# Optimization experiments

Measured on AMD Instinct MI355X. Metric: run time of the kernel, lower is better.

Reference implementation:

```python
import jax, jax.numpy as jnp
import numpy as np

B, T, DIM = 512, 243, 512
C = DIM // 2      # 256 channels per branch
CH = C // 2       # 128 hidden channels in ECL (cdiv=2)


def layer_norm(x, g, b, eps=1e-5):
    m = jnp.mean(x, axis=-1, keepdims=True)
    v = jnp.var(x, axis=-1, keepdims=True)
    return (x - m) * jax.lax.rsqrt(v + eps) * g + b


def gconv(x_btc, w):
    # grouped conv1d (groups=2), kernel 3, pad 1, no bias; x: [B,T,Cin], w: [Cout, Cin//2, 3]
    x = jnp.transpose(x_btc, (0, 2, 1))  # NCH
    y = jax.lax.conv_general_dilated(
        x, w, window_strides=(1,), padding=[(1, 1)],
        dimension_numbers=('NCH', 'OIH', 'NCH'), feature_group_count=2)
    return jnp.transpose(y, (0, 2, 1))


def setup_inputs() -> dict:
    key = jax.random.key(0)
    ks = jax.random.split(key, 4)
    F = (T + 1) // 2  # 122 == T//2+1 for odd T
    return {
        'x': jax.random.normal(ks[0], (B, T, DIM), dtype=jnp.float32),
        'lfilter': jax.random.normal(ks[1], (F, T // 2 + 1, 2), dtype=jnp.float32) * 0.02,
        'w1': jax.random.normal(ks[2], (CH, C // 2, 3), dtype=jnp.float32) * 0.05,
        'w2': jax.random.normal(ks[3], (C, CH // 2, 3), dtype=jnp.float32) * 0.05,
        'g1': jnp.ones((CH,), jnp.float32),
        'b1': jnp.zeros((CH,), jnp.float32),
        'g2': jnp.ones((C,), jnp.float32),
        'b2': jnp.zeros((C,), jnp.float32),
    }


def reference(x, lfilter, w1, w2, g1, b1, g2, b2):
    res, gate = jnp.split(x, 2, axis=-1)  # each [B, T, C]
    # GlobalFilter: rfft -> learned complex matmul over frequency axis -> irfft
    X = jnp.fft.rfft(res.astype(jnp.float32), n=T, axis=1, norm='ortho')  # [B, T//2+1, C] complex
    lf = lfilter[..., 0] + 1j * lfilter[..., 1]  # [(T+1)//2, T//2+1]
    X = jnp.einsum('fk,bkc->bfc', lf, X)
    res = jnp.fft.irfft(X, n=T, axis=1, norm='ortho')  # [B, T, C]
    # ECL gating branch
    h = gconv(gate, w1)                                  # [B, T, CH]
    h = jax.nn.gelu(layer_norm(h, g1, b1), approximate=False)
    h = gconv(h, w2)                                     # [B, T, C]
    h = jax.nn.sigmoid(layer_norm(h, g2, b2))
    gate = gate * h
    return jnp.concatenate([res, gate], axis=-1)
```

## Files before the change

kernel.cpp:

```cpp
#include <hip/hip_runtime.h>
#include <math.h>

typedef unsigned short ushort_t;
typedef unsigned int uint_t;
typedef __attribute__((ext_vector_type(8))) short short8v;
typedef __attribute__((ext_vector_type(4))) float f32x4;

#define BB   512
#define TT   243
#define DIMV 512
#define CC   256
#define CHH  128
#define FF   122
#define NKK  122

__device__ __forceinline__ float b2f(ushort_t u) {
  union { uint_t i; float f; } z; z.i = ((uint_t)u) << 16; return z.f;
}
__device__ __forceinline__ ushort_t f2b(float f) {
  union { float f; uint_t i; } z; z.f = f;
  uint_t r = (z.i + 0x7fffu + ((z.i >> 16) & 1u)) >> 16;
  return (ushort_t)r;
}
__device__ __forceinline__ uint_t pack2(float a, float b) {
  uint_t r;
  asm("v_cvt_pk_bf16_f32 %0, %1, %2" : "=v"(r) : "v"(a), "v"(b));
  return r;
}
__device__ __forceinline__ float gelu_f(float x) {
  float z = fabsf(x) * 0.70710678118654752f;
  float t = __builtin_amdgcn_rcpf(fmaf(0.3275911f, z, 1.0f));
  float p = fmaf(1.061405429f, t, -1.453152027f);
  p = fmaf(p, t, 1.421413741f);
  p = fmaf(p, t, -0.284496736f);
  p = fmaf(p, t, 0.254829592f);
  p = p * t;
  float e = __expf(-z * z);
  float erfa = 1.0f - p * e;
  float erfs = copysignf(erfa, x);
  return 0.5f * x * (1.0f + erfs);
}
__device__ __forceinline__ float sigmoid_f(float x) {
  return __builtin_amdgcn_rcpf(1.0f + __expf(-x));
}
union FragU { uint_t u[4]; short8v s; };


__global__ void k_compute_A(const float* __restrict__ lf, float* __restrict__ A) {
  __shared__ float2 tab[TT];
  int f = blockIdx.x;
  int tp = threadIdx.x;
  if (tp < TT) {
    float s, c;
    sincosf(6.28318530717958647692f * (float)tp / (float)TT, &s, &c);
    tab[tp] = make_float2(s, c);
  }
  __syncthreads();
  if (tp >= TT) return;
  float are = 0.f, aim = 0.f;
  int m = 0;
  const float* lrow = lf + (size_t)f * NKK * 2;
  for (int k = 0; k < NKK; ++k) {
    float2 sc = tab[m];
    float lr = lrow[2 * k], li = lrow[2 * k + 1];
    are = fmaf(lr, sc.y, fmaf(li, sc.x, are));
    aim = fmaf(li, sc.y, fmaf(-lr, sc.x, aim));
    m += tp; if (m >= TT) m -= TT;
  }
  A[(f * TT + tp) * 2 + 0] = are;
  A[(f * TT + tp) * 2 + 1] = aim;
}

__global__ void k_compute_M(const float* __restrict__ A, ushort_t* __restrict__ Ffrag) {
  __shared__ float2 tab[TT];
  int t = blockIdx.x;
  int tp = threadIdx.x;
  if (tp < TT) {
    float s, c;
    sincosf(6.28318530717958647692f * (float)tp / (float)TT, &s, &c);
    tab[tp] = make_float2(s, c);
  }
  __syncthreads();
  float val = 0.f;
  if (t < TT && tp < TT) {
    float acc = A[tp * 2 + 0];
    int m = t;
    for (int f = 1; f < FF; ++f) {
      float2 sc = tab[m];
      float ar = A[(f * TT + tp) * 2 + 0];
      float ai = A[(f * TT + tp) * 2 + 1];
      acc = fmaf(2.f * ar, sc.y, fmaf(-2.f * ai, sc.x, acc));
      m += t; if (m >= TT) m -= TT;
    }
    val = acc * (1.0f / (float)TT);
  }
  int kstep = tp >> 5, ko = tp & 31, p = ko >> 3, j = ko & 7;
  int mt = t >> 4, row = t & 15, lane = p * 16 + row;
  Ffrag[(((kstep * 16 + mt) * 64) + lane) * 8 + j] = f2b(val);
}

__global__ void k_prep_w(const float* __restrict__ w1, const float* __restrict__ w2,
                         ushort_t* __restrict__ w1f, ushort_t* __restrict__ w2f) {
  int q = blockIdx.x * 256 + threadIdx.x;
  if (q < 49152) {
    int j = q & 7, l = (q >> 3) & 63, ot = (q >> 9) & 3, rest = q >> 11;
    int ks = rest % 12, g = rest / 12;
    int o = ot * 16 + (l & 15);
    int k = ks * 32 + 8 * (l >> 4) + j;
    int dk = k >> 7, i = k & 127;
    w1f[q] = f2b(w1[(g * 64 + o) * 384 + i * 3 + dk]);
  } else if (q < 98304) {
    int q2 = q - 49152;
    int j = q2 & 7, l = (q2 >> 3) & 63, ot = (q2 >> 9) & 7, rest = q2 >> 12;
    int ks = rest % 6, g = rest / 6;
    int o = ot * 16 + (l & 15);
    int k = ks * 32 + 8 * (l >> 4) + j;
    int dk = k >> 6, i = k & 63;
    w2f[q2] = f2b(w2[(g * 128 + o) * 192 + i * 3 + dk]);
  }
}


#define RST 17
__global__ __launch_bounds__(256) void k_res(const float* __restrict__ x,
    const ushort_t* __restrict__ Ffrag, float* __restrict__ out) {
  __shared__ uint_t xs[2][64 * RST];
  int b = blockIdx.x >> 2, c0 = (blockIdx.x & 3) * 64;
  int tid = threadIdx.x, l = tid & 63, w = tid >> 6;
  const float* xb = x + (size_t)b * TT * DIMV + c0;
  const short8v* Fp = (const short8v*)Ffrag;

  f32x4 acc[4][4];
#pragma unroll
  for (int q = 0; q < 4; ++q)
#pragma unroll
    for (int m = 0; m < 4; ++m) acc[q][m] = (f32x4){0.f, 0.f, 0.f, 0.f};

  float v0[4], v1[4];
  int cc = tid & 63, kp0 = tid >> 6;

#pragma unroll
  for (int it = 0; it < 4; ++it) {
    int kp = kp0 + 4 * it, tp = 2 * kp;
    v0[it] = (tp < TT) ? xb[(size_t)tp * DIMV + cc] : 0.f;
    v1[it] = (tp + 1 < TT) ? xb[(size_t)(tp + 1) * DIMV + cc] : 0.f;
  }
#pragma unroll
  for (int it = 0; it < 4; ++it) xs[0][cc * RST + kp0 + 4 * it] = pack2(v0[it], v1[it]);
  __syncthreads();

  for (int ks = 0; ks < 8; ++ks) {
    int cur = ks & 1;
    if (ks < 7) {
#pragma unroll
      for (int it = 0; it < 4; ++it) {
        int kp = kp0 + 4 * it, tp = (ks + 1) * 32 + 2 * kp;
        v0[it] = (tp < TT) ? xb[(size_t)tp * DIMV + cc] : 0.f;
        v1[it] = (tp + 1 < TT) ? xb[(size_t)(tp + 1) * DIMV + cc] : 0.f;
      }
    }
    FragU bfr[4];
#pragma unroll
    for (int q = 0; q < 4; ++q) bfr[q].s = Fp[(ks * 16 + 4 * w + q) * 64 + l];
#pragma unroll
    for (int m = 0; m < 4; ++m) {
      FragU af;
      const uint_t* pp = &xs[cur][(16 * m + (l & 15)) * RST + 4 * (l >> 4)];
      af.u[0] = pp[0]; af.u[1] = pp[1]; af.u[2] = pp[2]; af.u[3] = pp[3];
#pragma unroll
      for (int q = 0; q < 4; ++q)
        acc[q][m] = __builtin_amdgcn_mfma_f32_16x16x32_bf16(af.s, bfr[q].s, acc[q][m], 0, 0, 0);
    }
    if (ks < 7) {
#pragma unroll
      for (int it = 0; it < 4; ++it) xs[cur ^ 1][cc * RST + kp0 + 4 * it] = pack2(v0[it], v1[it]);
    }
    __syncthreads();
  }

  float* ob = out + (size_t)b * TT * DIMV + c0;
#pragma unroll
  for (int q = 0; q < 4; ++q) {
    int t = (4 * w + q) * 16 + (l & 15);
    if (t < TT) {
#pragma unroll
      for (int m = 0; m < 4; ++m)
        *(f32x4*)&ob[(size_t)t * DIMV + 16 * m + 4 * (l >> 4)] = acc[q][m];
    }
  }
}


#define BT    32
#define NTIL  8
#define XROWS 36
#define XSTD  132
#define HROWS 34
#define HSTD  68

__global__ __launch_bounds__(256) void k_gate(const float* __restrict__ x,
    const ushort_t* __restrict__ w1f, const float* __restrict__ g1, const float* __restrict__ b1,
    const ushort_t* __restrict__ w2f, const float* __restrict__ g2, const float* __restrict__ b2,
    float* __restrict__ out) {
  __shared__ uint_t xs[XROWS * XSTD];
  __shared__ uint_t hs[HROWS * HSTD];
  __shared__ float red1s[4][48], red1q[4][48];
  __shared__ float red2s[4][32], red2q[4][32];
  int b = blockIdx.x >> 3, t0 = (blockIdx.x & 7) * BT;
  int tid = threadIdx.x, l = tid & 63, w = tid >> 6;
  int g = w >> 1, half = w & 1;

  const float* xb = x + (size_t)b * TT * DIMV + CC;
#pragma unroll 3
  for (int it = 0; it < 9; ++it) {
    int e = tid + it * 256;
    int r = e >> 6, cq = e & 63;
    int t = t0 - 2 + r;
    float4 v = make_float4(0.f, 0.f, 0.f, 0.f);
    if (t >= 0 && t < TT) v = *(const float4*)&xb[(size_t)t * DIMV + 4 * cq];
    *(uint2*)&xs[r * XSTD + 2 * cq] = make_uint2(pack2(v.x, v.y), pack2(v.z, v.w));
  }
  __syncthreads();

  const short8v* w1p = (const short8v*)w1f;
  int gdw = g * 64;
  f32x4 acc1[2][3];
#pragma unroll
  for (int a = 0; a < 2; ++a)
#pragma unroll
    for (int nt = 0; nt < 3; ++nt) acc1[a][nt] = (f32x4){0.f, 0.f, 0.f, 0.f};

  for (int ks = 0; ks < 12; ++ks) {
    short8v af[2];
#pragma unroll
    for (int a = 0; a < 2; ++a)
      af[a] = w1p[((g * 12 + ks) * 4 + half * 2 + a) * 64 + l];
    int dk = ks >> 2, i0dw = (ks & 3) * 16;
    FragU bf[3];
#pragma unroll
    for (int nt = 0; nt < 3; ++nt) {
      int row = (l & 15) + 16 * nt + dk;
      if (nt == 2) row = row > (XROWS - 1) ? (XROWS - 1) : row;
      const uint4* pp = (const uint4*)&xs[row * XSTD + gdw + i0dw + 4 * (l >> 4)];
      uint4 qv = *pp;
      bf[nt].u[0] = qv.x; bf[nt].u[1] = qv.y; bf[nt].u[2] = qv.z; bf[nt].u[3] = qv.w;
    }
#pragma unroll
    for (int a = 0; a < 2; ++a)
#pragma unroll
      for (int nt = 0; nt < 3; ++nt)
        acc1[a][nt] = __builtin_amdgcn_mfma_f32_16x16x32_bf16(af[a], bf[nt].s, acc1[a][nt], 0, 0, 0);
  }

#pragma unroll
  for (int nt = 0; nt < 3; ++nt) {
    float s = 0.f, s2 = 0.f;
#pragma unroll
    for (int a = 0; a < 2; ++a)
#pragma unroll
      for (int r = 0; r < 4; ++r) { float v = acc1[a][nt][r]; s += v; s2 += v * v; }
    s += __shfl_xor(s, 16); s += __shfl_xor(s, 32);
    s2 += __shfl_xor(s2, 16); s2 += __shfl_xor(s2, 32);
    if (l < 16) { red1s[w][l + 16 * nt] = s; red1q[w][l + 16 * nt] = s2; }
  }
  __syncthreads();

#pragma unroll
  for (int nt = 0; nt < 3; ++nt) {
    int c = (l & 15) + 16 * nt;
    if (c < HROWS) {
      int t_out = t0 - 1 + c;
      bool valid = (t_out >= 0 && t_out < TT);
      float S = red1s[0][c] + red1s[1][c] + red1s[2][c] + red1s[3][c];
      float S2 = red1q[0][c] + red1q[1][c] + red1q[2][c] + red1q[3][c];
      float mean = S * (1.f / 128.f);
      float var = S2 * (1.f / 128.f) - mean * mean;
      float rstd = rsqrtf(var + 1e-5f);
#pragma unroll
      for (int a = 0; a < 2; ++a) {
        int o0 = g * 64 + half * 32 + a * 16 + 4 * (l >> 4);
        float4 gg = *(const float4*)&g1[o0];
        float4 bb = *(const float4*)&b1[o0];
        float gv[4] = {gg.x, gg.y, gg.z, gg.w};
        float bv[4] = {bb.x, bb.y, bb.z, bb.w};
        float h4[4];
#pragma unroll
        for (int r = 0; r < 4; ++r) {
          float xn = (acc1[a][nt][r] - mean) * rstd * gv[r] + bv[r];
          h4[r] = valid ? gelu_f(xn) : 0.f;
        }
        *(uint2*)&hs[c * HSTD + (o0 >> 1)] =
            make_uint2(pack2(h4[0], h4[1]), pack2(h4[2], h4[3]));
      }
    }
  }
  __syncthreads();

  const short8v* w2p = (const short8v*)w2f;
  int gdw2 = g * 32;
  f32x4 acc2[4][2];
#pragma unroll
  for (int a = 0; a < 4; ++a)
#pragma unroll
    for (int nt = 0; nt < 2; ++nt) acc2[a][nt] = (f32x4){0.f, 0.f, 0.f, 0.f};

  for (int ks = 0; ks < 6; ++ks) {
    short8v af[4];
#pragma unroll
    for (int a = 0; a < 4; ++a)
      af[a] = w2p[((g * 6 + ks) * 8 + half * 4 + a) * 64 + l];
    int dk = ks >> 1, i0dw = (ks & 1) * 16;
    FragU bf[2];
#pragma unroll
    for (int nt = 0; nt < 2; ++nt) {
      int row = (l & 15) + 16 * nt + dk;
      const uint4* pp = (const uint4*)&hs[row * HSTD + gdw2 + i0dw + 4 * (l >> 4)];
      uint4 qv = *pp;
      bf[nt].u[0] = qv.x; bf[nt].u[1] = qv.y; bf[nt].u[2] = qv.z; bf[nt].u[3] = qv.w;
    }
#pragma unroll
    for (int a = 0; a < 4; ++a)
#pragma unroll
      for (int nt = 0; nt < 2; ++nt)
        acc2[a][nt] = __builtin_amdgcn_mfma_f32_16x16x32_bf16(af[a], bf[nt].s, acc2[a][nt], 0, 0, 0);
  }

#pragma unroll
  for (int nt = 0; nt < 2; ++nt) {
    float s = 0.f, s2 = 0.f;
#pragma unroll
    for (int a = 0; a < 4; ++a)
#pragma unroll
      for (int r = 0; r < 4; ++r) { float v = acc2[a][nt][r]; s += v; s2 += v * v; }
    s += __shfl_xor(s, 16); s += __shfl_xor(s, 32);
    s2 += __shfl_xor(s2, 16); s2 += __shfl_xor(s2, 32);
    if (l < 16) { red2s[w][l + 16 * nt] = s; red2q[w][l + 16 * nt] = s2; }
  }
  __syncthreads();

  float* ob = out + (size_t)b * TT * DIMV + CC;
#pragma unroll
  for (int nt = 0; nt < 2; ++nt) {
    int c = (l & 15) + 16 * nt;
    int t = t0 + c;
    if (t < TT) {
      float S = red2s[0][c] + red2s[1][c] + red2s[2][c] + red2s[3][c];
      float S2 = red2q[0][c] + red2q[1][c] + red2q[2][c] + red2q[3][c];
      float mean = S * (1.f / 256.f);
      float var = S2 * (1.f / 256.f) - mean * mean;
      float rstd = rsqrtf(var + 1e-5f);
      int xrow = c + 2;
#pragma unroll
      for (int a = 0; a < 4; ++a) {
        int o0 = g * 128 + (half * 4 + a) * 16 + 4 * (l >> 4);
        float4 gg = *(const float4*)&g2[o0];
        float4 bb = *(const float4*)&b2[o0];
        float gv[4] = {gg.x, gg.y, gg.z, gg.w};
        float bv[4] = {bb.x, bb.y, bb.z, bb.w};
        uint2 xv2 = *(const uint2*)&xs[xrow * XSTD + (o0 >> 1)];
        float xvv[4] = { b2f((ushort_t)(xv2.x & 0xffff)), b2f((ushort_t)(xv2.x >> 16)),
                         b2f((ushort_t)(xv2.y & 0xffff)), b2f((ushort_t)(xv2.y >> 16)) };
        f32x4 res;
#pragma unroll
        for (int r = 0; r < 4; ++r) {
          float xn = (acc2[a][nt][r] - mean) * rstd * gv[r] + bv[r];
          res[r] = xvv[r] * sigmoid_f(xn);
        }
        *(f32x4*)&ob[(size_t)t * DIMV + o0] = res;
      }
    }
  }
}


extern "C" void kernel_launch(void* const* d_in, const int* in_sizes, int n_in,
                              void* d_out, int out_size, void* d_ws, size_t ws_size,
                              hipStream_t stream) {
  const float* x  = (const float*)d_in[0];
  const float* lf = (const float*)d_in[1];
  const float* w1 = (const float*)d_in[2];
  const float* w2 = (const float*)d_in[3];
  const float* g1 = (const float*)d_in[4];
  const float* b1 = (const float*)d_in[5];
  const float* g2 = (const float*)d_in[6];
  const float* b2 = (const float*)d_in[7];
  float* out = (float*)d_out;

  char* ws = (char*)d_ws;
  float*    A     = (float*)(ws);
  ushort_t* Ffrag = (ushort_t*)(ws + 262144);
  ushort_t* w1f   = (ushort_t*)(ws + 393216);
  ushort_t* w2f   = (ushort_t*)(ws + 491520);

  k_compute_A<<<FF, 256, 0, stream>>>(lf, A);
  k_compute_M<<<256, 256, 0, stream>>>(A, Ffrag);
  k_prep_w<<<384, 256, 0, stream>>>(w1, w2, w1f, w2f);
  k_res<<<BB * 4, 256, 0, stream>>>(x, Ffrag, out);
  k_gate<<<BB * NTIL, 256, 0, stream>>>(x, w1f, g1, b1, w2f, g2, b2, out);
}
```

Measured before the change: 234.8 us.

## Fuse res and gate kernels into one interleaved launch; merge prep kernels

Merges the lfilter-to-A computation and the weight-fragment prep into a single launch. Combines the spectral-filter (res) and gating (gate) kernels into one kernel that assigns one res tile and two gate tiles per group of three blocks, sharing a union shared-memory buffer. This removes two launches and lets the MFMA-heavy res work overlap with the LayerNorm/GELU-heavy gate work on the same CUs, removing the tail between kernels. The cost is that every block reserves the larger shared-memory footprint and registers sized for the heavier path, and launch_bounds(256,4) may limit registers.

```diff
diff --git a/kernel.cpp b/kernel.cpp
--- a/kernel.cpp
+++ b/kernel.cpp
@@ -46,29 +46,52 @@
 union FragU { uint_t u[4]; short8v s; };
 
 
-__global__ void k_compute_A(const float* __restrict__ lf, float* __restrict__ A) {
+__global__ __launch_bounds__(256) void k_prep1(const float* __restrict__ lf, float* __restrict__ A,
+    const float* __restrict__ w1, const float* __restrict__ w2,
+    ushort_t* __restrict__ w1f, ushort_t* __restrict__ w2f) {
   __shared__ float2 tab[TT];
-  int f = blockIdx.x;
-  int tp = threadIdx.x;
-  if (tp < TT) {
-    float s, c;
-    sincosf(6.28318530717958647692f * (float)tp / (float)TT, &s, &c);
-    tab[tp] = make_float2(s, c);
-  }
-  __syncthreads();
-  if (tp >= TT) return;
-  float are = 0.f, aim = 0.f;
-  int m = 0;
-  const float* lrow = lf + (size_t)f * NKK * 2;
-  for (int k = 0; k < NKK; ++k) {
-    float2 sc = tab[m];
-    float lr = lrow[2 * k], li = lrow[2 * k + 1];
-    are = fmaf(lr, sc.y, fmaf(li, sc.x, are));
-    aim = fmaf(li, sc.y, fmaf(-lr, sc.x, aim));
-    m += tp; if (m >= TT) m -= TT;
-  }
-  A[(f * TT + tp) * 2 + 0] = are;
-  A[(f * TT + tp) * 2 + 1] = aim;
+  int bid = blockIdx.x;
+  if (bid < FF) {
+    int f = bid;
+    int tp = threadIdx.x;
+    if (tp < TT) {
+      float s, c;
+      sincosf(6.28318530717958647692f * (float)tp / (float)TT, &s, &c);
+      tab[tp] = make_float2(s, c);
+    }
+    __syncthreads();
+    if (tp >= TT) return;
+    float are = 0.f, aim = 0.f;
+    int m = 0;
+    const float* lrow = lf + (size_t)f * NKK * 2;
+    for (int k = 0; k < NKK; ++k) {
+      float2 sc = tab[m];
+      float lr = lrow[2 * k], li = lrow[2 * k + 1];
+      are = fmaf(lr, sc.y, fmaf(li, sc.x, are));
+      aim = fmaf(li, sc.y, fmaf(-lr, sc.x, aim));
+      m += tp; if (m >= TT) m -= TT;
+    }
+    A[(f * TT + tp) * 2 + 0] = are;
+    A[(f * TT + tp) * 2 + 1] = aim;
+  } else {
+    int q = (bid - FF) * 256 + threadIdx.x;
+    if (q < 49152) {
+      int j = q & 7, l = (q >> 3) & 63, ot = (q >> 9) & 3, rest = q >> 11;
+      int ks = rest % 12, g = rest / 12;
+      int o = ot * 16 + (l & 15);
+      int k = ks * 32 + 8 * (l >> 4) + j;
+      int dk = k >> 7, i = k & 127;
+      w1f[q] = f2b(w1[(g * 64 + o) * 384 + i * 3 + dk]);
+    } else if (q < 98304) {
+      int q2 = q - 49152;
+      int j = q2 & 7, l = (q2 >> 3) & 63, ot = (q2 >> 9) & 7, rest = q2 >> 12;
+      int ks = rest % 6, g = rest / 6;
+      int o = ot * 16 + (l & 15);
+      int k = ks * 32 + 8 * (l >> 4) + j;
+      int dk = k >> 6, i = k & 63;
+      w2f[q2] = f2b(w2[(g * 128 + o) * 192 + i * 3 + dk]);
+    }
+  }
 }
 
 __global__ void k_compute_M(const float* __restrict__ A, ushort_t* __restrict__ Ffrag) {
@@ -99,114 +122,97 @@
   Ffrag[(((kstep * 16 + mt) * 64) + lane) * 8 + j] = f2b(val);
 }
 
-__global__ void k_prep_w(const float* __restrict__ w1, const float* __restrict__ w2,
-                         ushort_t* __restrict__ w1f, ushort_t* __restrict__ w2f) {
-  int q = blockIdx.x * 256 + threadIdx.x;
-  if (q < 49152) {
-    int j = q & 7, l = (q >> 3) & 63, ot = (q >> 9) & 3, rest = q >> 11;
-    int ks = rest % 12, g = rest / 12;
-    int o = ot * 16 + (l & 15);
-    int k = ks * 32 + 8 * (l >> 4) + j;
-    int dk = k >> 7, i = k & 127;
-    w1f[q] = f2b(w1[(g * 64 + o) * 384 + i * 3 + dk]);
-  } else if (q < 98304) {
-    int q2 = q - 49152;
-    int j = q2 & 7, l = (q2 >> 3) & 63, ot = (q2 >> 9) & 7, rest = q2 >> 12;
-    int ks = rest % 6, g = rest / 6;
-    int o = ot * 16 + (l & 15);
-    int k = ks * 32 + 8 * (l >> 4) + j;
-    int dk = k >> 6, i = k & 63;
-    w2f[q2] = f2b(w2[(g * 128 + o) * 192 + i * 3 + dk]);
-  }
-}
-
-
-#define RST 17
-__global__ __launch_bounds__(256) void k_res(const float* __restrict__ x,
-    const ushort_t* __restrict__ Ffrag, float* __restrict__ out) {
-  __shared__ uint_t xs[2][64 * RST];
-  int b = blockIdx.x >> 2, c0 = (blockIdx.x & 3) * 64;
-  int tid = threadIdx.x, l = tid & 63, w = tid >> 6;
-  const float* xb = x + (size_t)b * TT * DIMV + c0;
-  const short8v* Fp = (const short8v*)Ffrag;
-
-  f32x4 acc[4][4];
-#pragma unroll
-  for (int q = 0; q < 4; ++q)
-#pragma unroll
-    for (int m = 0; m < 4; ++m) acc[q][m] = (f32x4){0.f, 0.f, 0.f, 0.f};
-
-  float v0[4], v1[4];
-  int cc = tid & 63, kp0 = tid >> 6;
-
-#pragma unroll
-  for (int it = 0; it < 4; ++it) {
-    int kp = kp0 + 4 * it, tp = 2 * kp;
-    v0[it] = (tp < TT) ? xb[(size_t)tp * DIMV + cc] : 0.f;
-    v1[it] = (tp + 1 < TT) ? xb[(size_t)(tp + 1) * DIMV + cc] : 0.f;
-  }
-#pragma unroll
-  for (int it = 0; it < 4; ++it) xs[0][cc * RST + kp0 + 4 * it] = pack2(v0[it], v1[it]);
-  __syncthreads();
-
-  for (int ks = 0; ks < 8; ++ks) {
-    int cur = ks & 1;
-    if (ks < 7) {
-#pragma unroll
-      for (int it = 0; it < 4; ++it) {
-        int kp = kp0 + 4 * it, tp = (ks + 1) * 32 + 2 * kp;
-        v0[it] = (tp < TT) ? xb[(size_t)tp * DIMV + cc] : 0.f;
-        v1[it] = (tp + 1 < TT) ? xb[(size_t)(tp + 1) * DIMV + cc] : 0.f;
-      }
-    }
-    FragU bfr[4];
-#pragma unroll
-    for (int q = 0; q < 4; ++q) bfr[q].s = Fp[(ks * 16 + 4 * w + q) * 64 + l];
-#pragma unroll
-    for (int m = 0; m < 4; ++m) {
-      FragU af;
-      const uint_t* pp = &xs[cur][(16 * m + (l & 15)) * RST + 4 * (l >> 4)];
-      af.u[0] = pp[0]; af.u[1] = pp[1]; af.u[2] = pp[2]; af.u[3] = pp[3];
-#pragma unroll
-      for (int q = 0; q < 4; ++q)
-        acc[q][m] = __builtin_amdgcn_mfma_f32_16x16x32_bf16(af.s, bfr[q].s, acc[q][m], 0, 0, 0);
-    }
-    if (ks < 7) {
-#pragma unroll
-      for (int it = 0; it < 4; ++it) xs[cur ^ 1][cc * RST + kp0 + 4 * it] = pack2(v0[it], v1[it]);
-    }
-    __syncthreads();
-  }
-
-  float* ob = out + (size_t)b * TT * DIMV + c0;
-#pragma unroll
-  for (int q = 0; q < 4; ++q) {
-    int t = (4 * w + q) * 16 + (l & 15);
-    if (t < TT) {
-#pragma unroll
-      for (int m = 0; m < 4; ++m)
-        *(f32x4*)&ob[(size_t)t * DIMV + 16 * m + 4 * (l >> 4)] = acc[q][m];
-    }
-  }
-}
-
-
+
+#define RST   17
 #define BT    32
 #define NTIL  8
 #define XROWS 36
 #define XSTD  132
 #define HROWS 34
 #define HSTD  68
-
-__global__ __launch_bounds__(256) void k_gate(const float* __restrict__ x,
+#define SMEM_DW 7704
+
+__device__ __forceinline__ void res_path(int rid, uint_t* smem,
+    const float* __restrict__ x, const ushort_t* __restrict__ Ffrag, float* __restrict__ out) {
+  uint_t* xs = smem;
+  int b = rid >> 2, c0 = (rid & 3) * 64;
+  int tid = threadIdx.x, l = tid & 63, w = tid >> 6;
+  const float* xb = x + (size_t)b * TT * DIMV + c0;
+  const short8v* Fp = (const short8v*)Ffrag;
+
+  f32x4 acc[4][4];
+#pragma unroll
+  for (int q = 0; q < 4; ++q)
+#pragma unroll
+    for (int m = 0; m < 4; ++m) acc[q][m] = (f32x4){0.f, 0.f, 0.f, 0.f};
+
+  float v0[4], v1[4];
+  int cc = tid & 63, kp0 = tid >> 6;
+
+#pragma unroll
+  for (int it = 0; it < 4; ++it) {
+    int kp = kp0 + 4 * it, tp = 2 * kp;
+    v0[it] = (tp < TT) ? xb[(size_t)tp * DIMV + cc] : 0.f;
+    v1[it] = (tp + 1 < TT) ? xb[(size_t)(tp + 1) * DIMV + cc] : 0.f;
+  }
+#pragma unroll
+  for (int it = 0; it < 4; ++it) xs[cc * RST + kp0 + 4 * it] = pack2(v0[it], v1[it]);
+  __syncthreads();
+
+  for (int ks = 0; ks < 8; ++ks) {
+    int cur = ks & 1;
+    if (ks < 7) {
+#pragma unroll
+      for (int it = 0; it < 4; ++it) {
+        int kp = kp0 + 4 * it, tp = (ks + 1) * 32 + 2 * kp;
+        v0[it] = (tp < TT) ? xb[(size_t)tp * DIMV + cc] : 0.f;
+        v1[it] = (tp + 1 < TT) ? xb[(size_t)(tp + 1) * DIMV + cc] : 0.f;
+      }
+    }
+    FragU bfr[4];
+#pragma unroll
+    for (int q = 0; q < 4; ++q) bfr[q].s = Fp[(ks * 16 + 4 * w + q) * 64 + l];
+#pragma unroll
+    for (int m = 0; m < 4; ++m) {
+      FragU af;
+      const uint_t* pp = &xs[cur * (64 * RST) + (16 * m + (l & 15)) * RST + 4 * (l >> 4)];
+      af.u[0] = pp[0]; af.u[1] = pp[1]; af.u[2] = pp[2]; af.u[3] = pp[3];
+#pragma unroll
+      for (int q = 0; q < 4; ++q)
+        acc[q][m] = __builtin_amdgcn_mfma_f32_16x16x32_bf16(af.s, bfr[q].s, acc[q][m], 0, 0, 0);
+    }
+    if (ks < 7) {
+#pragma unroll
+      for (int it = 0; it < 4; ++it)
+        xs[(cur ^ 1) * (64 * RST) + cc * RST + kp0 + 4 * it] = pack2(v0[it], v1[it]);
+    }
+    __syncthreads();
+  }
+
+  float* ob = out + (size_t)b * TT * DIMV + c0;
+#pragma unroll
+  for (int q = 0; q < 4; ++q) {
+    int t = (4 * w + q) * 16 + (l & 15);
+    if (t < TT) {
+#pragma unroll
+      for (int m = 0; m < 4; ++m)
+        *(f32x4*)&ob[(size_t)t * DIMV + 16 * m + 4 * (l >> 4)] = acc[q][m];
+    }
+  }
+}
+
+__device__ __forceinline__ void gate_path(int gid, uint_t* smem,
+    const float* __restrict__ x,
     const ushort_t* __restrict__ w1f, const float* __restrict__ g1, const float* __restrict__ b1,
     const ushort_t* __restrict__ w2f, const float* __restrict__ g2, const float* __restrict__ b2,
     float* __restrict__ out) {
-  __shared__ uint_t xs[XROWS * XSTD];
-  __shared__ uint_t hs[HROWS * HSTD];
-  __shared__ float red1s[4][48], red1q[4][48];
-  __shared__ float red2s[4][32], red2q[4][32];
-  int b = blockIdx.x >> 3, t0 = (blockIdx.x & 7) * BT;
+  uint_t* xs = smem;
+  uint_t* hs = smem + XROWS * XSTD;
+  float* red1s = (float*)(hs + HROWS * HSTD);
+  float* red1q = red1s + 4 * 48;
+  float* red2s = red1q + 4 * 48;
+  float* red2q = red2s + 4 * 32;
+  int b = gid >> 3, t0 = (gid & 7) * BT;
   int tid = threadIdx.x, l = tid & 63, w = tid >> 6;
   int g = w >> 1, half = w & 1;
 
@@ -261,7 +267,7 @@
       for (int r = 0; r < 4; ++r) { float v = acc1[a][nt][r]; s += v; s2 += v * v; }
     s += __shfl_xor(s, 16); s += __shfl_xor(s, 32);
     s2 += __shfl_xor(s2, 16); s2 += __shfl_xor(s2, 32);
-    if (l < 16) { red1s[w][l + 16 * nt] = s; red1q[w][l + 16 * nt] = s2; }
+    if (l < 16) { red1s[w * 48 + l + 16 * nt] = s; red1q[w * 48 + l + 16 * nt] = s2; }
   }
   __syncthreads();
 
@@ -271,8 +277,8 @@
     if (c < HROWS) {
       int t_out = t0 - 1 + c;
       bool valid = (t_out >= 0 && t_out < TT);
-      float S = red1s[0][c] + red1s[1][c] + red1s[2][c] + red1s[3][c];
-      float S2 = red1q[0][c] + red1q[1][c] + red1q[2][c] + red1q[3][c];
+      float S = red1s[0 * 48 + c] + red1s[1 * 48 + c] + red1s[2 * 48 + c] + red1s[3 * 48 + c];
+      float S2 = red1q[0 * 48 + c] + red1q[1 * 48 + c] + red1q[2 * 48 + c] + red1q[3 * 48 + c];
       float mean = S * (1.f / 128.f);
       float var = S2 * (1.f / 128.f) - mean * mean;
       float rstd = rsqrtf(var + 1e-5f);
@@ -334,7 +340,7 @@
       for (int r = 0; r < 4; ++r) { float v = acc2[a][nt][r]; s += v; s2 += v * v; }
     s += __shfl_xor(s, 16); s += __shfl_xor(s, 32);
     s2 += __shfl_xor(s2, 16); s2 += __shfl_xor(s2, 32);
-    if (l < 16) { red2s[w][l + 16 * nt] = s; red2q[w][l + 16 * nt] = s2; }
+    if (l < 16) { red2s[w * 32 + l + 16 * nt] = s; red2q[w * 32 + l + 16 * nt] = s2; }
   }
   __syncthreads();
 
@@ -344,8 +350,8 @@
     int c = (l & 15) + 16 * nt;
     int t = t0 + c;
     if (t < TT) {
-      float S = red2s[0][c] + red2s[1][c] + red2s[2][c] + red2s[3][c];
-      float S2 = red2q[0][c] + red2q[1][c] + red2q[2][c] + red2q[3][c];
+      float S = red2s[0 * 32 + c] + red2s[1 * 32 + c] + red2s[2 * 32 + c] + red2s[3 * 32 + c];
+      float S2 = red2q[0 * 32 + c] + red2q[1 * 32 + c] + red2q[2 * 32 + c] + red2q[3 * 32 + c];
       float mean = S * (1.f / 256.f);
       float var = S2 * (1.f / 256.f) - mean * mean;
       float rstd = rsqrtf(var + 1e-5f);
@@ -369,6 +375,21 @@
         *(f32x4*)&ob[(size_t)t * DIMV + o0] = res;
       }
     }
+  }
+}
+
+__global__ __launch_bounds__(256, 4) void k_main(const float* __restrict__ x,
+    const ushort_t* __restrict__ Ffrag,
+    const ushort_t* __restrict__ w1f, const float* __restrict__ g1, const float* __restrict__ b1,
+    const ushort_t* __restrict__ w2f, const float* __restrict__ g2, const float* __restrict__ b2,
+    float* __restrict__ out) {
+  __shared__ uint_t smem[SMEM_DW];
+  int bid = blockIdx.x;
+  int k = bid / 3, r = bid - 3 * k;
+  if (r == 0) {
+    res_path(k, smem, x, Ffrag, out);
+  } else {
+    gate_path(2 * k + (r - 1), smem, x, w1f, g1, b1, w2f, g2, b2, out);
   }
 }
 
@@ -392,9 +413,7 @@
   ushort_t* w1f   = (ushort_t*)(ws + 393216);
   ushort_t* w2f   = (ushort_t*)(ws + 491520);
 
-  k_compute_A<<<FF, 256, 0, stream>>>(lf, A);
+  k_prep1<<<FF + 384, 256, 0, stream>>>(lf, A, w1, w2, w1f, w2f);
   k_compute_M<<<256, 256, 0, stream>>>(A, Ffrag);
-  k_prep_w<<<384, 256, 0, stream>>>(w1, w2, w1f, w2f);
-  k_res<<<BB * 4, 256, 0, stream>>>(x, Ffrag, out);
-  k_gate<<<BB * NTIL, 256, 0, stream>>>(x, w1f, g1, b1, w2f, g2, b2, out);
-}
+  k_main<<<BB * 4 * 3, 256, 0, stream>>>(x, Ffrag, w1f, g1, b1, w2f, g2, b2, out);
+}
```

After: 211.5 us. 1.11x faster.
